# Optimization experiments

Hardware: AMD Instinct MI355X
Metric: run time of the kernel (lower is better)

Reference implementation:

```python
import jax, jax.numpy as jnp
import numpy as np


def setup_inputs() -> dict:
    key = jax.random.key(0)
    k1, k2, k3, k4 = jax.random.split(key, 4)
    n_smps, n_fcns, d_in, d_out = 16384, 2048, 32, 32
    GAIN = 1e-5  # xavier gain used by init_wts / init_offsets
    x = jax.random.normal(k1, (n_smps, d_in), dtype=jnp.float32)
    ctrs = jax.random.normal(k2, (n_fcns, d_in), dtype=jnp.float32)
    wts = jax.random.normal(k3, (n_fcns, d_in, d_out), dtype=jnp.float32) * GAIN
    offsets = jax.random.normal(k4, (n_fcns, d_out), dtype=jnp.float32) * GAIN
    return {"x": x, "ctrs": ctrs, "wts": wts, "offsets": offsets, "k": 4}


def reference(x, ctrs, wts, offsets, k):
    # --- knn_do equivalent (done under no_grad in torch) ---
    # squared Euclidean distance: (n_smps, n_fcns)
    x_sg = jax.lax.stop_gradient(x)
    c_sg = jax.lax.stop_gradient(ctrs)
    d2 = (jnp.sum(x_sg * x_sg, axis=1, keepdims=True)
          - 2.0 * (x_sg @ c_sg.T)
          + jnp.sum(c_sg * c_sg, axis=1)[None, :])
    _, idx = jax.lax.top_k(-d2, k)  # (n_smps, k), nearest centers

    # --- gather per-neighbor local linear models ---
    sel_wts = wts[idx]        # (n_smps, k, d_in, d_out)
    sel_ctrs = ctrs[idx]      # (n_smps, k, d_in)
    sel_offs = offsets[idx]   # (n_smps, k, d_out)

    applied_wts = jnp.sum(sel_wts, axis=1)  # (n_smps, d_in, d_out)
    # offsets minus sum over neighbors/d_in of wts * ctrs
    applied_offsets = (jnp.sum(sel_offs, axis=1)
                       - jnp.einsum('nkde,nkd->ne', sel_wts, sel_ctrs))
    # y = x @ applied_wts + applied_offsets, per sample
    y = jnp.einsum('nde,nd->ne', applied_wts, x) + applied_offsets
    return y
```

## Files before the change

kernel.cpp:

```cpp
#include <hip/hip_runtime.h>
#include <math.h>

typedef short bf16x8 __attribute__((ext_vector_type(8)));
typedef float f32x4  __attribute__((ext_vector_type(4)));

#define N_SMPS 16384
#define N_FCNS 2048
#define D_IN 32
#define D_OUT 32
#define KNN 4
#define SPLITS 4
#define CPS 512
#define TILES 32
#define POOL 48
#define SMP 16

__device__ __forceinline__ unsigned umin_u(unsigned a, unsigned b) { return a < b ? a : b; }
__device__ __forceinline__ unsigned umax_u(unsigned a, unsigned b) { return a > b ? a : b; }

__device__ __forceinline__ unsigned short bf16_rne(float f) {
  unsigned b = __float_as_uint(f);
  unsigned r = b + 0x7FFFu + ((b >> 16) & 1u);
  return (unsigned short)(r >> 16);
}

#define OFF_XH   0u
#define OFF_CH   1048576u
#define OFF_HB   (OFF_CH + 131072u)
#define OFF_WB   (OFF_HB + 8192u)

#define NX4 (N_SMPS * D_IN / 4)
#define NC4 (N_FCNS * D_IN / 4)
#define NW4 (N_FCNS * D_IN * D_OUT / 4)
#define NTOT (NX4 + NC4 + NW4)

__global__ __launch_bounds__(256) void k_prep(
    const float* __restrict__ x, const float* __restrict__ ctrs,
    const float* __restrict__ wts,
    unsigned short* __restrict__ xh, unsigned short* __restrict__ ch,
    unsigned short* __restrict__ wb, float* __restrict__ hb)
{
  const int gt = blockIdx.x * 256 + threadIdx.x;
  const float* src; unsigned short* dst; int i4;
  if (gt < NX4)            { src = x;    dst = xh; i4 = gt; }
  else if (gt < NX4 + NC4) { src = ctrs; dst = ch; i4 = gt - NX4; }
  else                     { src = wts;  dst = wb; i4 = gt - (NX4 + NC4); }
  float4 v = ((const float4*)src)[i4];
  ushort4 o;
  o.x = bf16_rne(v.x); o.y = bf16_rne(v.y);
  o.z = bf16_rne(v.z); o.w = bf16_rne(v.w);
  ((ushort4*)dst)[i4] = o;

  if (gt < N_FCNS) {
    const float4* cp4 = (const float4*)(ctrs + (size_t)gt * D_IN);
    float a = 0.f;
    #pragma unroll
    for (int q = 0; q < 8; ++q) {
      float4 c = cp4[q];
      a += c.x * c.x + c.y * c.y + c.z * c.z + c.w * c.w;
    }
    hb[gt] = -0.5f * a;
  }
}

__global__ __launch_bounds__(256) void k_mega(
    const unsigned short* __restrict__ xh, const unsigned short* __restrict__ ch,
    const float* __restrict__ hb,
    const float* __restrict__ x, const float* __restrict__ ctrs,
    const unsigned short* __restrict__ wb, const float* __restrict__ offs,
    float* __restrict__ y)
{
  __shared__ __align__(16) char u_mem[16640];
  __shared__ float    s_hb[SPLITS * CPS];
  __shared__ unsigned s_pool[SMP][POOL];
  __shared__ double   s_pd2[SMP][POOL];
  __shared__ int      s_pix[SMP][POOL];
  __shared__ int      s_sel[SMP][KNN];

  unsigned* s_cand = (unsigned*)u_mem;
  float*    s_diff = (float*)u_mem;
  float4*   s_part = (float4*)(u_mem + 8448);

  const int tid = threadIdx.x;
  const int lane = tid & 63;
  const int w = __builtin_amdgcn_readfirstlane(tid >> 6);
  const int col = lane & 15;
  const int quad = lane >> 4;
  const int sbase = blockIdx.x * SMP;
  const int nbase0 = w * CPS;

  #pragma unroll
  for (int r = 0; r < CPS / 64; ++r)
    s_hb[nbase0 + r * 64 + lane] = hb[nbase0 + r * 64 + lane];

  const bf16x8 ah =
      *(const bf16x8*)(xh + (size_t)(sbase + col) * D_IN + quad * 8);

  unsigned ls[4][4];
  #pragma unroll
  for (int r = 0; r < 4; ++r)
    #pragma unroll
    for (int e = 0; e < 4; ++e) ls[r][e] = 0u;

  const unsigned short* chb =
      ch + (size_t)nbase0 * D_IN + (size_t)col * D_IN + quad * 8;
  #define BLOAD(t) (*(const bf16x8*)(chb + (size_t)(t) * 16 * D_IN))
  #define HLOAD(t) (s_hb[nbase0 + (t) * 16 + col])

  __syncthreads();

  bf16x8 bh[4];
  float  hv[4];
  #pragma unroll
  for (int p = 0; p < 4; ++p) { bh[p] = BLOAD(p); hv[p] = HLOAD(p); }

  for (int t = 0; t < TILES; t += 4) {
    #pragma unroll
    for (int p = 0; p < 4; ++p) {
      {
        f32x4 acc = {0.f, 0.f, 0.f, 0.f};
        acc = __builtin_amdgcn_mfma_f32_16x16x32_bf16(ah, bh[p], acc, 0, 0, 0);
        const unsigned tc = (unsigned)((t + p) * 16 + col);
        const float hvv = hv[p];
        #pragma unroll
        for (int r = 0; r < 4; ++r) {
          const float uu = acc[r] + hvv;
          unsigned b = __float_as_uint(uu);
          unsigned m = b ^ ((unsigned)((int)b >> 31) | 0x80000000u);
          unsigned key = (m & 0xFFFFFE00u) | tc;
          unsigned t0 = umin_u(ls[r][0], key); ls[r][0] = umax_u(ls[r][0], key);
          unsigned t1 = umin_u(ls[r][1], t0);  ls[r][1] = umax_u(ls[r][1], t0);
          unsigned t2 = umin_u(ls[r][2], t1);  ls[r][2] = umax_u(ls[r][2], t1);
          ls[r][3] = umax_u(ls[r][3], t2);
        }
      }
      const int tn = (t + 4 + p) & (TILES - 1);
      bh[p] = BLOAD(tn);
      hv[p] = HLOAD(tn);
    }
  }
  #undef BLOAD
  #undef HLOAD

  #pragma unroll
  for (int r = 0; r < 4; ++r) {
    const int row = quad * 4 + r;
    *(uint4*)&s_cand[(((w * 16) + row) * 16 + col) * 4] =
        make_uint4(ls[r][0], ls[r][1], ls[r][2], ls[r][3]);
  }
  __syncthreads();

  if (tid < 128) {
    const int sl = tid >> 3;
    const int g  = tid & 7;
    const int wv = g >> 1;
    const int chh = (g & 1) * 8;
    unsigned q0 = 0, q1 = 0, q2 = 0, q3 = 0, q4 = 0, q5 = 0;
    #pragma unroll
    for (int c2 = 0; c2 < 8; ++c2) {
      uint4 kv = *(const uint4*)&s_cand[(((wv * 16) + sl) * 16 + chh + c2) * 4];
      unsigned ks[4] = {kv.x, kv.y, kv.z, kv.w};
      #pragma unroll
      for (int e = 0; e < 4; ++e) {
        unsigned key = ks[e];
        unsigned t0 = umin_u(q0, key); q0 = umax_u(q0, key);
        unsigned t1 = umin_u(q1, t0);  q1 = umax_u(q1, t0);
        unsigned t2 = umin_u(q2, t1);  q2 = umax_u(q2, t1);
        unsigned t3 = umin_u(q3, t2);  q3 = umax_u(q3, t2);
        unsigned t4 = umin_u(q4, t3);  q4 = umax_u(q4, t3);
        q5 = umax_u(q5, t4);
      }
    }
    unsigned* op = &s_pool[sl][g * 6];
    op[0] = q0; op[1] = q1; op[2] = q2;
    op[3] = q3; op[4] = q4; op[5] = q5;
  }
  __syncthreads();

  for (int c = tid; c < SMP * POOL; c += 256) {
    const int sl = c / POOL;
    const int p = c - sl * POOL;
    const unsigned key = s_pool[sl][p];
    const int wv = p / 12;
    const int j = wv * CPS + (int)(key & 0x1FFu);
    const float4* xp4 = (const float4*)(x + (size_t)(sbase + sl) * D_IN);
    const float4* cp4 = (const float4*)(ctrs + (size_t)j * D_IN);
    double d2a = 0.0, d2b = 0.0;
    #pragma unroll
    for (int q = 0; q < 8; ++q) {
      float4 cv = cp4[q];
      float4 xv = xp4[q];
      double df0 = (double)xv.x - (double)cv.x;
      double df1 = (double)xv.y - (double)cv.y;
      double df2 = (double)xv.z - (double)cv.z;
      double df3 = (double)xv.w - (double)cv.w;
      d2a = fma(df0, df0, d2a);
      d2b = fma(df1, df1, d2b);
      d2a = fma(df2, df2, d2a);
      d2b = fma(df3, df3, d2b);
    }
    s_pd2[sl][p] = d2a + d2b;
    s_pix[sl][p] = j;
  }
  __syncthreads();

  if (tid < SMP) {
    double bd[4]; int b4[4];
    #pragma unroll
    for (int e = 0; e < 4; ++e) { bd[e] = 1e300; b4[e] = 0x7fffffff; }
    for (int m = 0; m < POOL; ++m) {
      const double d2 = s_pd2[tid][m];
      const int j = s_pix[tid][m];
      bool ins = (d2 < bd[3]) || (d2 == bd[3] && j < b4[3]);
      if (ins) {
        bd[3] = d2; b4[3] = j;
        #pragma unroll
        for (int q = 3; q > 0; --q) {
          bool sw = (bd[q] < bd[q - 1]) ||
                    (bd[q] == bd[q - 1] && b4[q] < b4[q - 1]);
          if (sw) {
            double td = bd[q]; bd[q] = bd[q - 1]; bd[q - 1] = td;
            int    tj = b4[q]; b4[q] = b4[q - 1]; b4[q - 1] = tj;
          }
        }
      }
    }
    #pragma unroll
    for (int q = 0; q < 4; ++q) s_sel[tid][q] = b4[q];
  }
  __syncthreads();

  #pragma unroll
  for (int r = 0; r < SMP * KNN * D_IN / 256; ++r) {
    int v = r * 256 + tid;
    int d = v & 31; int p = v >> 5;
    int sl = p >> 2; int j = p & 3;
    int f = s_sel[sl][j];
    s_diff[(sl * KNN + j) * (D_IN + 1) + d] =
        x[(size_t)(sbase + sl) * D_IN + d] - ctrs[(size_t)f * D_IN + d];
  }
  __syncthreads();

  #pragma unroll
  for (int r = 0; r < 2; ++r) {
    const int slot = r * 256 + tid;
    const int sl = slot >> 5;
    const int j  = (slot >> 3) & 3;
    const int eq = slot & 7;
    const int f = s_sel[sl][j];
    const uint2* wp = (const uint2*)(wb + (size_t)f * (D_IN * D_OUT));
    float4 acc = ((const float4*)(offs + (size_t)f * D_OUT))[eq];
    #pragma unroll
    for (int d = 0; d < D_IN; ++d) {
      uint2 wv = wp[d * 8 + eq];
      float w0 = __uint_as_float(wv.x << 16);
      float w1 = __uint_as_float(wv.x & 0xFFFF0000u);
      float w2 = __uint_as_float(wv.y << 16);
      float w3 = __uint_as_float(wv.y & 0xFFFF0000u);
      float xc = s_diff[(sl * KNN + j) * (D_IN + 1) + d];
      acc.x = fmaf(xc, w0, acc.x);
      acc.y = fmaf(xc, w1, acc.y);
      acc.z = fmaf(xc, w2, acc.z);
      acc.w = fmaf(xc, w3, acc.w);
    }
    s_part[(sl * KNN + j) * 8 + eq] = acc;
  }
  __syncthreads();

  #pragma unroll
  for (int r = 0; r < 2; ++r) {
    const int slot = r * 256 + tid;
    const int sl = slot >> 5;
    const int j  = (slot >> 3) & 3;
    const int eq = slot & 7;
    if (j == 0) {
      float4 a = s_part[(sl * KNN + 0) * 8 + eq];
      float4 b = s_part[(sl * KNN + 1) * 8 + eq];
      float4 c = s_part[(sl * KNN + 2) * 8 + eq];
      float4 e = s_part[(sl * KNN + 3) * 8 + eq];
      float4 o;
      o.x = (a.x + b.x) + (c.x + e.x);
      o.y = (a.y + b.y) + (c.y + e.y);
      o.z = (a.z + b.z) + (c.z + e.z);
      o.w = (a.w + b.w) + (c.w + e.w);
      ((float4*)(y + (size_t)(sbase + sl) * D_OUT))[eq] = o;
    }
  }
}

extern "C" void kernel_launch(void* const* d_in, const int* in_sizes, int n_in,
                              void* d_out, int out_size, void* d_ws, size_t ws_size,
                              hipStream_t stream) {
  const float* x    = (const float*)d_in[0];
  const float* ctrs = (const float*)d_in[1];
  const float* wts  = (const float*)d_in[2];
  const float* offs = (const float*)d_in[3];
  float* y = (float*)d_out;

  char* ws = (char*)d_ws;
  unsigned short* xh = (unsigned short*)(ws + OFF_XH);
  unsigned short* ch = (unsigned short*)(ws + OFF_CH);
  float*          hb = (float*)(ws + OFF_HB);
  unsigned short* wb = (unsigned short*)(ws + OFF_WB);

  k_prep<<<NTOT / 256, 256, 0, stream>>>(x, ctrs, wts, xh, ch, wb, hb);
  k_mega<<<N_SMPS / SMP, 256, 0, stream>>>(xh, ch, hb, x, ctrs, wb, offs, y);
}
```

Before: 110.2 us.

## Split mega kernel and bucket sample-neighbor pairs by center for weight reuse

Breaks the fused kernel into top-k, refine, counting-sort (scan/place), apply and reduce kernels. Sample-neighbor pairs are grouped by selected center so that each apply block reads mostly the same weight matrices, aiming to raise cache reuse of the 2048x32x32 weights instead of scattered gathers. The cost is more kernel launches, global round-trips for the pool, index, list and partial buffers, atomics for counting, and a single-block scan.

```diff
diff --git a/kernel.cpp b/kernel.cpp
--- a/kernel.cpp
+++ b/kernel.cpp
@@ -14,6 +14,7 @@
 #define TILES 32
 #define POOL 48
 #define SMP 16
+#define NPAIR (N_SMPS * KNN)
 
 __device__ __forceinline__ unsigned umin_u(unsigned a, unsigned b) { return a < b ? a : b; }
 __device__ __forceinline__ unsigned umax_u(unsigned a, unsigned b) { return a > b ? a : b; }
@@ -26,8 +27,15 @@
 
 #define OFF_XH   0u
 #define OFF_CH   1048576u
-#define OFF_HB   (OFF_CH + 131072u)
-#define OFF_WB   (OFF_HB + 8192u)
+#define OFF_HB   1179648u
+#define OFF_WB   1187840u
+#define OFF_POOL 5382144u
+#define OFF_IDX  8527872u
+#define OFF_CNT  8790016u
+#define OFF_CNT2 8798208u
+#define OFF_BASE 8806400u
+#define OFF_LIST 8814848u
+#define OFF_PART 9076992u
 
 #define NX4 (N_SMPS * D_IN / 4)
 #define NC4 (N_FCNS * D_IN / 4)
@@ -38,7 +46,8 @@
     const float* __restrict__ x, const float* __restrict__ ctrs,
     const float* __restrict__ wts,
     unsigned short* __restrict__ xh, unsigned short* __restrict__ ch,
-    unsigned short* __restrict__ wb, float* __restrict__ hb)
+    unsigned short* __restrict__ wb, float* __restrict__ hb,
+    int* __restrict__ cnt, int* __restrict__ cnt2)
 {
   const int gt = blockIdx.x * 256 + threadIdx.x;
   const float* src; unsigned short* dst; int i4;
@@ -60,26 +69,17 @@
       a += c.x * c.x + c.y * c.y + c.z * c.z + c.w * c.w;
     }
     hb[gt] = -0.5f * a;
-  }
-}
-
-__global__ __launch_bounds__(256) void k_mega(
+    cnt[gt] = 0;
+    cnt2[gt] = 0;
+  }
+}
+
+__global__ __launch_bounds__(256) void k_topk(
     const unsigned short* __restrict__ xh, const unsigned short* __restrict__ ch,
-    const float* __restrict__ hb,
-    const float* __restrict__ x, const float* __restrict__ ctrs,
-    const unsigned short* __restrict__ wb, const float* __restrict__ offs,
-    float* __restrict__ y)
-{
-  __shared__ __align__(16) char u_mem[16640];
+    const float* __restrict__ hb, unsigned* __restrict__ pool)
+{
+  __shared__ unsigned s_cand[SPLITS][16][16][4];
   __shared__ float    s_hb[SPLITS * CPS];
-  __shared__ unsigned s_pool[SMP][POOL];
-  __shared__ double   s_pd2[SMP][POOL];
-  __shared__ int      s_pix[SMP][POOL];
-  __shared__ int      s_sel[SMP][KNN];
-
-  unsigned* s_cand = (unsigned*)u_mem;
-  float*    s_diff = (float*)u_mem;
-  float4*   s_part = (float4*)(u_mem + 8448);
 
   const int tid = threadIdx.x;
   const int lane = tid & 63;
@@ -145,7 +145,7 @@
   #pragma unroll
   for (int r = 0; r < 4; ++r) {
     const int row = quad * 4 + r;
-    *(uint4*)&s_cand[(((w * 16) + row) * 16 + col) * 4] =
+    *(uint4*)&s_cand[w][row][col][0] =
         make_uint4(ls[r][0], ls[r][1], ls[r][2], ls[r][3]);
   }
   __syncthreads();
@@ -158,7 +158,7 @@
     unsigned q0 = 0, q1 = 0, q2 = 0, q3 = 0, q4 = 0, q5 = 0;
     #pragma unroll
     for (int c2 = 0; c2 < 8; ++c2) {
-      uint4 kv = *(const uint4*)&s_cand[(((wv * 16) + sl) * 16 + chh + c2) * 4];
+      uint4 kv = *(const uint4*)&s_cand[wv][sl][chh + c2][0];
       unsigned ks[4] = {kv.x, kv.y, kv.z, kv.w};
       #pragma unroll
       for (int e = 0; e < 4; ++e) {
@@ -171,16 +171,26 @@
         q5 = umax_u(q5, t4);
       }
     }
-    unsigned* op = &s_pool[sl][g * 6];
+    unsigned* op = pool + (size_t)(sbase + sl) * POOL + g * 6;
     op[0] = q0; op[1] = q1; op[2] = q2;
     op[3] = q3; op[4] = q4; op[5] = q5;
   }
-  __syncthreads();
+}
+
+__global__ __launch_bounds__(256) void k_refine(
+    const float* __restrict__ x, const float* __restrict__ ctrs,
+    const unsigned* __restrict__ pool, int* __restrict__ idx_out,
+    int* __restrict__ cnt)
+{
+  __shared__ double s_pd2[SMP][POOL];
+  __shared__ int    s_pix[SMP][POOL];
+  const int tid = threadIdx.x;
+  const int sbase = blockIdx.x * SMP;
 
   for (int c = tid; c < SMP * POOL; c += 256) {
     const int sl = c / POOL;
     const int p = c - sl * POOL;
-    const unsigned key = s_pool[sl][p];
+    const unsigned key = pool[(size_t)(sbase + sl) * POOL + p];
     const int wv = p / 12;
     const int j = wv * CPS + (int)(key & 0x1FFu);
     const float4* xp4 = (const float4*)(x + (size_t)(sbase + sl) * D_IN);
@@ -226,28 +236,85 @@
       }
     }
     #pragma unroll
-    for (int q = 0; q < 4; ++q) s_sel[tid][q] = b4[q];
-  }
-  __syncthreads();
-
-  #pragma unroll
-  for (int r = 0; r < SMP * KNN * D_IN / 256; ++r) {
-    int v = r * 256 + tid;
-    int d = v & 31; int p = v >> 5;
-    int sl = p >> 2; int j = p & 3;
-    int f = s_sel[sl][j];
-    s_diff[(sl * KNN + j) * (D_IN + 1) + d] =
-        x[(size_t)(sbase + sl) * D_IN + d] - ctrs[(size_t)f * D_IN + d];
+    for (int q = 0; q < 4; ++q) {
+      idx_out[(sbase + tid) * KNN + q] = b4[q];
+      atomicAdd(&cnt[b4[q]], 1);
+    }
+  }
+}
+
+__global__ __launch_bounds__(256) void k_scan(
+    const int* __restrict__ cnt, int* __restrict__ base)
+{
+  __shared__ int s_sum[256];
+  const int tid = threadIdx.x;
+  int loc[8]; int acc = 0;
+  #pragma unroll
+  for (int q = 0; q < 8; ++q) { loc[q] = acc; acc += cnt[tid * 8 + q]; }
+  s_sum[tid] = acc;
+  __syncthreads();
+  #pragma unroll
+  for (int off = 1; off < 256; off <<= 1) {
+    int v = (tid >= off) ? s_sum[tid - off] : 0;
+    __syncthreads();
+    s_sum[tid] += v;
+    __syncthreads();
+  }
+  const int pre = (tid == 0) ? 0 : s_sum[tid - 1];
+  #pragma unroll
+  for (int q = 0; q < 8; ++q) base[tid * 8 + q] = pre + loc[q];
+  if (tid == 255) base[N_FCNS] = pre + acc;
+}
+
+__global__ __launch_bounds__(256) void k_place(
+    const int* __restrict__ idx, const int* __restrict__ base,
+    int* __restrict__ cnt2, int* __restrict__ list)
+{
+  const int t = blockIdx.x * 256 + threadIdx.x;
+  const int f = idx[t];
+  const int pos = base[f] + atomicAdd(&cnt2[f], 1);
+  list[pos] = t;
+}
+
+__global__ __launch_bounds__(256) void k_apply2(
+    const float* __restrict__ x, const float* __restrict__ ctrs,
+    const unsigned short* __restrict__ wb, const float* __restrict__ offs,
+    const int* __restrict__ idx, const int* __restrict__ list,
+    float* __restrict__ part)
+{
+  __shared__ float s_diff[64][D_IN + 1];
+  __shared__ int   s_t[64];
+  __shared__ int   s_f[64];
+  const int tid = threadIdx.x;
+  const int pbase = blockIdx.x * 64;
+
+  if (tid < 64) {
+    const int t = list[pbase + tid];
+    s_t[tid] = t;
+    s_f[tid] = idx[t];
+  }
+  __syncthreads();
+
+  {
+    const int i = tid >> 2, seg = tid & 3;
+    const int s = s_t[i] >> 2, f = s_f[i];
+    const float4* xp = (const float4*)(x + (size_t)s * D_IN) + seg * 2;
+    const float4* cp = (const float4*)(ctrs + (size_t)f * D_IN) + seg * 2;
+    float4 xv0 = xp[0], xv1 = xp[1], cv0 = cp[0], cv1 = cp[1];
+    float* dp = &s_diff[i][seg * 8];
+    dp[0] = xv0.x - cv0.x; dp[1] = xv0.y - cv0.y;
+    dp[2] = xv0.z - cv0.z; dp[3] = xv0.w - cv0.w;
+    dp[4] = xv1.x - cv1.x; dp[5] = xv1.y - cv1.y;
+    dp[6] = xv1.z - cv1.z; dp[7] = xv1.w - cv1.w;
   }
   __syncthreads();
 
   #pragma unroll
   for (int r = 0; r < 2; ++r) {
-    const int slot = r * 256 + tid;
-    const int sl = slot >> 5;
-    const int j  = (slot >> 3) & 3;
-    const int eq = slot & 7;
-    const int f = s_sel[sl][j];
+    const int task = r * 256 + tid;
+    const int pr = task >> 3;
+    const int eq = task & 7;
+    const int f = s_f[pr];
     const uint2* wp = (const uint2*)(wb + (size_t)f * (D_IN * D_OUT));
     float4 acc = ((const float4*)(offs + (size_t)f * D_OUT))[eq];
     #pragma unroll
@@ -257,35 +324,30 @@
       float w1 = __uint_as_float(wv.x & 0xFFFF0000u);
       float w2 = __uint_as_float(wv.y << 16);
       float w3 = __uint_as_float(wv.y & 0xFFFF0000u);
-      float xc = s_diff[(sl * KNN + j) * (D_IN + 1) + d];
+      float xc = s_diff[pr][d];
       acc.x = fmaf(xc, w0, acc.x);
       acc.y = fmaf(xc, w1, acc.y);
       acc.z = fmaf(xc, w2, acc.z);
       acc.w = fmaf(xc, w3, acc.w);
     }
-    s_part[(sl * KNN + j) * 8 + eq] = acc;
-  }
-  __syncthreads();
-
-  #pragma unroll
-  for (int r = 0; r < 2; ++r) {
-    const int slot = r * 256 + tid;
-    const int sl = slot >> 5;
-    const int j  = (slot >> 3) & 3;
-    const int eq = slot & 7;
-    if (j == 0) {
-      float4 a = s_part[(sl * KNN + 0) * 8 + eq];
-      float4 b = s_part[(sl * KNN + 1) * 8 + eq];
-      float4 c = s_part[(sl * KNN + 2) * 8 + eq];
-      float4 e = s_part[(sl * KNN + 3) * 8 + eq];
-      float4 o;
-      o.x = (a.x + b.x) + (c.x + e.x);
-      o.y = (a.y + b.y) + (c.y + e.y);
-      o.z = (a.z + b.z) + (c.z + e.z);
-      o.w = (a.w + b.w) + (c.w + e.w);
-      ((float4*)(y + (size_t)(sbase + sl) * D_OUT))[eq] = o;
-    }
-  }
+    ((float4*)(part + (size_t)s_t[pr] * D_OUT))[eq] = acc;
+  }
+}
+
+__global__ __launch_bounds__(256) void k_reduce(
+    const float* __restrict__ part, float* __restrict__ y)
+{
+  const int t = blockIdx.x * 256 + threadIdx.x;
+  const int s = t >> 3;
+  const int c4 = t & 7;
+  const float4* p = (const float4*)(part + (size_t)s * 4 * D_OUT) + c4;
+  float4 a = p[0], b = p[8], c = p[16], e = p[24];
+  float4 o;
+  o.x = (a.x + b.x) + (c.x + e.x);
+  o.y = (a.y + b.y) + (c.y + e.y);
+  o.z = (a.z + b.z) + (c.z + e.z);
+  o.w = (a.w + b.w) + (c.w + e.w);
+  ((float4*)(y + (size_t)s * D_OUT))[c4] = o;
 }
 
 extern "C" void kernel_launch(void* const* d_in, const int* in_sizes, int n_in,
@@ -302,7 +364,20 @@
   unsigned short* ch = (unsigned short*)(ws + OFF_CH);
   float*          hb = (float*)(ws + OFF_HB);
   unsigned short* wb = (unsigned short*)(ws + OFF_WB);
-
-  k_prep<<<NTOT / 256, 256, 0, stream>>>(x, ctrs, wts, xh, ch, wb, hb);
-  k_mega<<<N_SMPS / SMP, 256, 0, stream>>>(xh, ch, hb, x, ctrs, wb, offs, y);
-}
+  unsigned*     pool = (unsigned*)(ws + OFF_POOL);
+  int*          idxb = (int*)(ws + OFF_IDX);
+  int*           cnt = (int*)(ws + OFF_CNT);
+  int*          cnt2 = (int*)(ws + OFF_CNT2);
+  int*          base = (int*)(ws + OFF_BASE);
+  int*          list = (int*)(ws + OFF_LIST);
+  float*        part = (float*)(ws + OFF_PART);
+
+  k_prep<<<NTOT / 256, 256, 0, stream>>>(x, ctrs, wts, xh, ch, wb, hb,
+                                         cnt, cnt2);
+  k_topk<<<N_SMPS / SMP, 256, 0, stream>>>(xh, ch, hb, pool);
+  k_refine<<<N_SMPS / SMP, 256, 0, stream>>>(x, ctrs, pool, idxb, cnt);
+  k_scan<<<1, 256, 0, stream>>>(cnt, base);
+  k_place<<<NPAIR / 256, 256, 0, stream>>>(idxb, base, cnt2, list);
+  k_apply2<<<NPAIR / 64, 256, 0, stream>>>(x, ctrs, wb, offs, idxb, list, part);
+  k_reduce<<<(N_SMPS * 8) / 256, 256, 0, stream>>>(part, y);
+}
```

New measurement: 155.1 us. 40.7% more time.
